# Optimization experiments

Measured on AMD Instinct MI355X. Metric: run time of the kernel, lower is better.

## Reference

```python
import jax, jax.numpy as jnp
import numpy as np

NUM_JOINTS = 24
NUM_THETAS = NUM_JOINTS * 3  # 72
NUM_VERTS = 6890
NUM_BETAS = 10
BATCH = 512

SMPL_PARENTS = np.array([0, 0, 0, 0, 1, 2, 3, 4, 5, 6, 7, 8, 9, 9, 9,
                         12, 13, 14, 16, 17, 18, 19, 20, 21], dtype=np.int32)


def setup_inputs() -> dict:
    key = jax.random.key(0)
    ks = jax.random.split(key, 6)
    x = jax.random.normal(ks[0], (BATCH, NUM_THETAS + NUM_BETAS), dtype=jnp.float32) * 0.3
    v_template = jax.random.normal(ks[1], (NUM_VERTS, 3), dtype=jnp.float32) * 0.3
    shapedirs = jax.random.normal(ks[2], (NUM_BETAS, NUM_VERTS * 3), dtype=jnp.float32) * 0.01
    posedirs = jax.random.normal(ks[3], (207, NUM_VERTS * 3), dtype=jnp.float32) * 0.001
    Jr = jax.random.uniform(ks[4], (NUM_VERTS, NUM_JOINTS), dtype=jnp.float32)
    J_regressor = Jr / jnp.sum(Jr, axis=0, keepdims=True)
    W = jax.random.uniform(ks[5], (NUM_VERTS, NUM_JOINTS), dtype=jnp.float32)
    lbs_weights = W / jnp.sum(W, axis=1, keepdims=True)  # rows sum to 1 (skinning weights)
    parents = jnp.asarray(SMPL_PARENTS)
    return {"x": x, "v_template": v_template, "shapedirs": shapedirs,
            "J_regressor": J_regressor, "posedirs": posedirs,
            "lbs_weights": lbs_weights, "parents": parents}


def batch_rodrigues(theta):
    # theta: [N,3] axis-angle -> [N,3,3] rotation matrices
    angle = jnp.linalg.norm(theta + 1e-8, axis=1, keepdims=True)  # [N,1]
    r = theta / angle                                              # [N,3] unit axis
    cos = jnp.cos(angle)[..., None]                                # [N,1,1]
    sin = jnp.sin(angle)[..., None]
    outer = r[:, :, None] * r[:, None, :]                          # [N,3,3]
    rx, ry, rz = r[:, 0], r[:, 1], r[:, 2]
    zero = jnp.zeros_like(rx)
    K = jnp.stack([zero, -rz, ry,
                   rz, zero, -rx,
                   -ry, rx, zero], axis=1).reshape(-1, 3, 3)       # skew-symmetric
    eye = jnp.eye(3, dtype=theta.dtype)
    return cos * eye + (1.0 - cos) * outer + sin * K


def global_rigid_transformation(Rs, J, parents):
    # Rs: [B,24,3,3], J: [B,24,3] -> A: [B,24,4,4]
    B = Rs.shape[0]
    dtype = Rs.dtype
    bottom = jnp.broadcast_to(jnp.array([0, 0, 0, 1], dtype=dtype), (B, 1, 4))

    def make_A(R, t):  # R:[B,3,3], t:[B,3]
        Rt = jnp.concatenate([R, t[:, :, None]], axis=2)  # [B,3,4]
        return jnp.concatenate([Rt, bottom], axis=1)       # [B,4,4]

    parents = np.asarray(parents)
    results = [make_A(Rs[:, 0], J[:, 0])]
    for i in range(1, NUM_JOINTS):
        t_rel = J[:, i] - J[:, parents[i]]
        A_here = make_A(Rs[:, i], t_rel)
        results.append(jnp.matmul(results[parents[i]], A_here))
    results = jnp.stack(results, axis=1)  # [B,24,4,4]

    Js_w0 = jnp.concatenate([J, jnp.zeros((B, NUM_JOINTS, 1), dtype=dtype)], axis=2)  # [B,24,4]
    init_bone = jnp.einsum('bjpq,bjq->bjp', results, Js_w0)                           # [B,24,4]
    A = results - jnp.pad(init_bone[..., None], ((0, 0), (0, 0), (0, 0), (3, 0)))
    return A


def reference(x, v_template, shapedirs, J_regressor, posedirs, lbs_weights, parents):
    B = x.shape[0]
    thetas = x[:, :NUM_THETAS]
    betas = x[:, NUM_THETAS:]

    # shape blendshapes
    v_shaped = (betas @ shapedirs).reshape(B, NUM_VERTS, 3) + v_template  # [B,V,3]

    J = jnp.einsum('bvc,vj->bjc', v_shaped, J_regressor)  # [B,24,3]

    # pose rotations + pose blendshapes
    Rs = batch_rodrigues(thetas.reshape(-1, 3)).reshape(B, NUM_JOINTS, 3, 3)
    pose_feature = (Rs[:, 1:] - jnp.eye(3, dtype=x.dtype)).reshape(B, 207)
    v_posed = (pose_feature @ posedirs).reshape(B, NUM_VERTS, 3) + v_shaped

    # kinematic chain
    A = global_rigid_transformation(Rs, J, parents)  # [B,24,4,4]

    # linear blend skinning
    T = jnp.einsum('vj,bjpq->bvpq', lbs_weights, A)  # [B,V,4,4]
    v_posed_homo = jnp.concatenate(
        [v_posed, jnp.ones((B, NUM_VERTS, 1), dtype=x.dtype)], axis=2)  # [B,V,4]
    verts = jnp.einsum('bvpq,bvq->bvp', T, v_posed_homo)[:, :, :3]
    return verts
```

## Files before the change

kernel.cpp:

```cpp
#include <hip/hip_runtime.h>

#define NUM_JOINTS 24
#define NUM_VERTS  6890
#define NUM_COORDS (NUM_VERTS * 3)
#define NUM_BETAS  10
#define KTOT       217
#define KPAD       224
#define BATCH      512
#define VPAD       6912

#define WS_SJP  0
#define WS_XBF  85536
#define WS_DBF  142880
#define WS_WHBF 2465312
#define WS_AH   2575904
#define WS_AL   2706976

typedef __attribute__((ext_vector_type(8))) short short8;
typedef __attribute__((ext_vector_type(4))) float f32x4;

__device__ inline unsigned short f2bf(float f) {
    union { float f; unsigned u; } c; c.f = f;
    unsigned u = c.u;
    u += 0x7fffu + ((u >> 16) & 1u);
    return (unsigned short)(u >> 16);
}
__device__ inline float bf2f(unsigned short h) {
    union { unsigned u; float f; } c; c.u = ((unsigned)h) << 16;
    return c.f;
}

struct PBShm {
    float Rs[4][24][9];
    float Jl[4][24][3];
    float Rg[4][24][9];
    float tg[4][24][3];
    float As[4][24][12];
};

__global__ __launch_bounds__(256) void k_prep(const float* __restrict__ Jr,
                                              const float* __restrict__ sd,
                                              const float* __restrict__ pd,
                                              const float* __restrict__ vt,
                                              const float* __restrict__ w,
                                              float* __restrict__ ws) {
    __shared__ __align__(16) unsigned char smem[28928];
    const int t   = blockIdx.x;
    const int tid = threadIdx.x;
    unsigned short* whbf = (unsigned short*)(ws + WS_WHBF);
    unsigned short* dbf  = (unsigned short*)(ws + WS_DBF);

    if (t < 27) {
        const int v = t * 256 + tid;
        const bool ok = (v < NUM_VERTS);
        unsigned short row[32];
        #pragma unroll
        for (int j = 0; j < 32; ++j)
            row[j] = f2bf((ok && j < 24) ? w[v * 24 + j] : 0.f);
        #pragma unroll
        for (int i = 0; i < 4; ++i)
            *(float4*)(whbf + (size_t)v * 32 + i * 8) = *(const float4*)(&row[i * 8]);
    } else if (t < 351) {
        unsigned* L = (unsigned*)smem;
        const int c0   = (t - 27) * 64;
        const int lane = tid & 63;
        const int grp  = tid >> 6;
        const int c    = c0 + lane;
        const bool cv  = (c < NUM_COORDS);
        #pragma unroll 4
        for (int i = 0; i < 28; ++i) {
            const int p  = i * 4 + grp;
            const int k0 = 2 * p, k1 = k0 + 1;
            float v0 = 0.f, v1 = 0.f;
            if (cv) {
                v0 = (k0 < 10) ? sd[(size_t)k0 * NUM_COORDS + c]
                   : (k0 < KTOT) ? pd[(size_t)(k0 - 10) * NUM_COORDS + c] : 0.f;
                v1 = (k1 < 10) ? sd[(size_t)k1 * NUM_COORDS + c]
                   : (k1 < KTOT) ? pd[(size_t)(k1 - 10) * NUM_COORDS + c] : 0.f;
            }
            L[lane * 113 + p] = (unsigned)f2bf(v0) | ((unsigned)f2bf(v1) << 16);
        }
        __syncthreads();
        #pragma unroll
        for (int i = 0; i < 7; ++i) {
            const int idx = i * 256 + tid;
            const int row = idx / 28;
            const int q   = idx % 28;
            uint4 val;
            val.x = L[row * 113 + q * 4 + 0];
            val.y = L[row * 113 + q * 4 + 1];
            val.z = L[row * 113 + q * 4 + 2];
            val.w = L[row * 113 + q * 4 + 3];
            *(uint4*)(dbf + (size_t)(c0 + row) * KPAD + q * 8) = val;
        }
    } else {
        float* Jl = (float*)smem;
        float* S  = (float*)smem + 64 * 25;
        const int strip = t - 351;
        const int v0 = strip * 64;
        #pragma unroll
        for (int i = 0; i < 6; ++i) {
            const int idx = i * 256 + tid;
            const int v = idx / 24, j = idx % 24;
            Jl[v * 25 + j] = (v0 + v < NUM_VERTS) ? Jr[(size_t)(v0 + v) * 24 + j] : 0.f;
        }
        #pragma unroll
        for (int i = 0; i < 9; ++i) {
            const int idx = i * 256 + tid;
            if (idx < 33 * 64) {
                const int s = idx / 64, v = idx % 64;
                float val = 0.f;
                if (v0 + v < NUM_VERTS) {
                    if (s < 30) val = sd[(size_t)(s / 3) * NUM_COORDS + (size_t)(v0 + v) * 3 + (s % 3)];
                    else        val = vt[(size_t)(v0 + v) * 3 + (s - 30)];
                }
                S[s * 64 + v] = val;
            }
        }
        __syncthreads();
        float* wsp = ws + WS_SJP + (size_t)strip * 792;
        for (int o = tid; o < 792; o += 256) {
            const int s = o / 24, j = o % 24;
            float sum = 0.f;
            #pragma unroll 8
            for (int v = 0; v < 64; ++v)
                sum += S[s * 64 + v] * Jl[v * 25 + j];
            wsp[o] = sum;
        }
    }
}

__global__ __launch_bounds__(256) void k_pb(const float* __restrict__ x,
                                            const int* __restrict__ parents,
                                            float* __restrict__ ws) {
    __shared__ PBShm P;
    __shared__ float SJf[792];
    unsigned short* xbf = (unsigned short*)(ws + WS_XBF);
    unsigned short* ahi = (unsigned short*)(ws + WS_AH);
    unsigned short* alo = (unsigned short*)(ws + WS_AL);
    const int tid = threadIdx.x;

    {
        const float* wsp = ws + WS_SJP;
        for (int o = tid; o < 792; o += 256) {
            float sum = 0.f;
            for (int s2 = 0; s2 < 108; ++s2)
                sum += wsp[(size_t)s2 * 792 + o];
            SJf[o] = sum;
        }
    }
    __syncthreads();

    const int sub  = tid >> 6;
    const int lane = tid & 63;
    const int b = blockIdx.x * 4 + sub;
    const float* row = x + b * (NUM_BETAS + 72);

    if (lane < 24) {
        const int j = lane;
        const float t0 = row[3 * j + 0], t1 = row[3 * j + 1], t2 = row[3 * j + 2];
        const float a0 = t0 + 1e-8f, a1 = t1 + 1e-8f, a2 = t2 + 1e-8f;
        const float angle = sqrtf(a0 * a0 + a1 * a1 + a2 * a2);
        const float inv = 1.0f / angle;
        const float rx = t0 * inv, ry = t1 * inv, rz = t2 * inv;
        const float c = cosf(angle), sn = sinf(angle), o = 1.f - c;
        float R[9];
        R[0] = c + o * rx * rx;       R[1] = o * rx * ry - sn * rz; R[2] = o * rx * rz + sn * ry;
        R[3] = o * rx * ry + sn * rz; R[4] = c + o * ry * ry;       R[5] = o * ry * rz - sn * rx;
        R[6] = o * rx * rz - sn * ry; R[7] = o * ry * rz + sn * rx; R[8] = c + o * rz * rz;
        #pragma unroll
        for (int i = 0; i < 9; ++i) P.Rs[sub][j][i] = R[i];
        #pragma unroll
        for (int c3 = 0; c3 < 3; ++c3) {
            float s = SJf[(30 + c3) * 24 + j];
            #pragma unroll
            for (int k = 0; k < NUM_BETAS; ++k)
                s += row[72 + k] * SJf[(k * 3 + c3) * 24 + j];
            P.Jl[sub][j][c3] = s;
        }
        if (j >= 1) {
            #pragma unroll
            for (int i = 0; i < 9; ++i) {
                const float pf = R[i] - ((i == 0 || i == 4 || i == 8) ? 1.f : 0.f);
                xbf[(size_t)b * KPAD + 10 + (j - 1) * 9 + i] = f2bf(pf);
            }
        }
    }
    if (lane < NUM_BETAS) xbf[(size_t)b * KPAD + lane] = f2bf(row[72 + lane]);
    if (lane == 63) {
        #pragma unroll
        for (int k = KTOT; k < KPAD; ++k) xbf[(size_t)b * KPAD + k] = 0;
    }
    __syncthreads();

    if (lane == 0) {
        float Rg[24][9], tg[24][3];
        #pragma unroll
        for (int q = 0; q < 9; ++q) { Rg[0][q] = P.Rs[sub][0][q]; P.Rg[sub][0][q] = Rg[0][q]; }
        #pragma unroll
        for (int c3 = 0; c3 < 3; ++c3) { tg[0][c3] = P.Jl[sub][0][c3]; P.tg[sub][0][c3] = tg[0][c3]; }

        #pragma unroll
        for (int i = 1; i < 24; ++i) {
            constexpr int PAR[24] = {0, 0, 0, 0, 1, 2, 3, 4, 5, 6, 7, 8,
                                     9, 9, 9, 12, 13, 14, 16, 17, 18, 19, 20, 21};
            const int p = PAR[i];
            float Rsl[9];
            #pragma unroll
            for (int q = 0; q < 9; ++q) Rsl[q] = P.Rs[sub][i][q];
            float tmp[9];
            #pragma unroll
            for (int r = 0; r < 3; ++r)
                #pragma unroll
                for (int cc = 0; cc < 3; ++cc)
                    tmp[r * 3 + cc] = Rg[p][r * 3 + 0] * Rsl[0 + cc] +
                                      Rg[p][r * 3 + 1] * Rsl[3 + cc] +
                                      Rg[p][r * 3 + 2] * Rsl[6 + cc];
            #pragma unroll
            for (int q = 0; q < 9; ++q) { Rg[i][q] = tmp[q]; P.Rg[sub][i][q] = tmp[q]; }
            const float tr0 = P.Jl[sub][i][0] - P.Jl[sub][p][0];
            const float tr1 = P.Jl[sub][i][1] - P.Jl[sub][p][1];
            const float tr2 = P.Jl[sub][i][2] - P.Jl[sub][p][2];
            #pragma unroll
            for (int r = 0; r < 3; ++r) {
                tg[i][r] = Rg[p][r * 3 + 0] * tr0 + Rg[p][r * 3 + 1] * tr1 +
                           Rg[p][r * 3 + 2] * tr2 + tg[p][r];
                P.tg[sub][i][r] = tg[i][r];
            }
        }
    }
    __syncthreads();

    if (lane < 24) {
        const int j = lane;
        #pragma unroll
        for (int r = 0; r < 3; ++r) {
            const float tt = P.tg[sub][j][r] - (P.Rg[sub][j][r * 3 + 0] * P.Jl[sub][j][0] +
                                                P.Rg[sub][j][r * 3 + 1] * P.Jl[sub][j][1] +
                                                P.Rg[sub][j][r * 3 + 2] * P.Jl[sub][j][2]);
            P.As[sub][j][r * 4 + 0] = P.Rg[sub][j][r * 3 + 0];
            P.As[sub][j][r * 4 + 1] = P.Rg[sub][j][r * 3 + 1];
            P.As[sub][j][r * 4 + 2] = P.Rg[sub][j][r * 3 + 2];
            P.As[sub][j][r * 4 + 3] = tt;
        }
    }
    __syncthreads();

    if (lane < 32) {
        const int r = lane >> 1;
        const int half = lane & 1;
        unsigned short hi[16], lo[16];
        #pragma unroll
        for (int i = 0; i < 16; ++i) {
            const int j = half * 16 + i;
            float v = 0.f;
            if (r < 12 && j < 24) v = P.As[sub][j][r];
            const unsigned short h = f2bf(v);
            hi[i] = h;
            lo[i] = f2bf(v - bf2f(h));
        }
        unsigned short* dh = ahi + ((size_t)b * 16 + r) * 32 + half * 16;
        unsigned short* dl = alo + ((size_t)b * 16 + r) * 32 + half * 16;
        #pragma unroll
        for (int i = 0; i < 2; ++i) {
            *(float4*)(dh + i * 8) = *(const float4*)(&hi[i * 8]);
            *(float4*)(dl + i * 8) = *(const float4*)(&lo[i * 8]);
        }
    }
}

__global__ __launch_bounds__(256) void k_fused(const float* __restrict__ vt,
                                               float* __restrict__ out,
                                               float* __restrict__ ws) {
    __shared__ __align__(16) float VP[64 * 194];
    __shared__ __align__(16) unsigned char U[20480];
    unsigned short* Xs = (unsigned short*)U;
    float*          Tsf = (float*)U;

    const unsigned short* dbf  = (const unsigned short*)(ws + WS_DBF);
    const unsigned short* xbf  = (const unsigned short*)(ws + WS_XBF);
    const unsigned short* whbf = (const unsigned short*)(ws + WS_WHBF);
    const unsigned short* ahi  = (const unsigned short*)(ws + WS_AH);
    const unsigned short* alo  = (const unsigned short*)(ws + WS_AL);

    const int tid  = threadIdx.x;
    const int wave = tid >> 6;
    const int lane = tid & 63;
    const int col  = lane & 15;
    const int quad = lane >> 4;
    const int c0   = blockIdx.x * 192;
    const int b0   = blockIdx.y * 64;

    short8 bfrag[3][7];
    float vtl[3];
    #pragma unroll
    for (int nt = 0; nt < 3; ++nt) {
        const int nc = c0 + wave * 48 + nt * 16 + col;
        const unsigned short* brow = dbf + (size_t)nc * KPAD + quad * 8;
        #pragma unroll
        for (int kb = 0; kb < 7; ++kb)
            bfrag[nt][kb] = *(const short8*)(brow + kb * 32);
        vtl[nt] = (nc < NUM_COORDS) ? vt[nc] : 0.f;
    }

    for (int chunk = 0; chunk < 2; ++chunk) {
        const int m0 = b0 + chunk * 32;
        __syncthreads();
        #pragma unroll
        for (int i = 0; i < 4; ++i) {
            const int c = tid + i * 256;
            if (c < 32 * 28) {
                const int r = c / 28, off = c % 28;
                *(float4*)(&Xs[r * 232 + off * 8]) =
                    *(const float4*)(xbf + (size_t)(m0 + r) * KPAD + off * 8);
            }
        }
        __syncthreads();

        #pragma unroll
        for (int mt = 0; mt < 2; ++mt) {
            const unsigned short* arow = &Xs[(mt * 16 + col) * 232 + quad * 8];
            f32x4 acc[3] = {{0.f,0.f,0.f,0.f},{0.f,0.f,0.f,0.f},{0.f,0.f,0.f,0.f}};
            #pragma unroll
            for (int kb = 0; kb < 7; ++kb) {
                const short8 af = *(const short8*)(arow + kb * 32);
                #pragma unroll
                for (int nt = 0; nt < 3; ++nt)
                    acc[nt] = __builtin_amdgcn_mfma_f32_16x16x32_bf16(af, bfrag[nt][kb], acc[nt], 0, 0, 0);
            }
            #pragma unroll
            for (int nt = 0; nt < 3; ++nt) {
                const int cc = wave * 48 + nt * 16 + col;
                #pragma unroll
                for (int r = 0; r < 4; ++r)
                    VP[(chunk * 32 + mt * 16 + quad * 4 + r) * 194 + cc] = acc[nt][r] + vtl[nt];
            }
        }
    }
    __syncthreads();

    const int v0 = blockIdx.x * 64;
    short8 wfrag[4];
    #pragma unroll
    for (int mt = 0; mt < 4; ++mt)
        wfrag[mt] = *(const short8*)(whbf + (size_t)(v0 + mt * 16 + col) * 32 + quad * 8);

    float* ts = Tsf + wave * (64 * 20);
    const int vv = v0 + lane;
    const bool vok = (vv < NUM_VERTS);

    for (int nt = wave; nt < 64; nt += 4) {
        const int b = b0 + nt;
        const short8 bh = *(const short8*)(ahi + ((size_t)b * 16 + col) * 32 + quad * 8);
        const short8 bl = *(const short8*)(alo + ((size_t)b * 16 + col) * 32 + quad * 8);

        f32x4 acc2[4];
        #pragma unroll
        for (int mt = 0; mt < 4; ++mt) {
            f32x4 z = {0.f, 0.f, 0.f, 0.f};
            z = __builtin_amdgcn_mfma_f32_16x16x32_bf16(wfrag[mt], bh, z, 0, 0, 0);
            z = __builtin_amdgcn_mfma_f32_16x16x32_bf16(wfrag[mt], bl, z, 0, 0, 0);
            acc2[mt] = z;
        }
        #pragma unroll
        for (int mt = 0; mt < 4; ++mt)
            #pragma unroll
            for (int r = 0; r < 4; ++r)
                ts[(mt * 16 + quad * 4 + r) * 20 + col] = acc2[mt][r];

        const f32x4 t0 = *(const f32x4*)(ts + lane * 20 + 0);
        const f32x4 t1 = *(const f32x4*)(ts + lane * 20 + 4);
        const f32x4 t2 = *(const f32x4*)(ts + lane * 20 + 8);

        const float h0 = VP[nt * 194 + lane * 3 + 0];
        const float h1 = VP[nt * 194 + lane * 3 + 1];
        const float h2 = VP[nt * 194 + lane * 3 + 2];

        if (vok) {
            float* orow = out + (size_t)b * NUM_COORDS + (size_t)vv * 3;
            __builtin_nontemporal_store(t0[0] * h0 + t0[1] * h1 + t0[2] * h2 + t0[3], orow + 0);
            __builtin_nontemporal_store(t1[0] * h0 + t1[1] * h1 + t1[2] * h2 + t1[3], orow + 1);
            __builtin_nontemporal_store(t2[0] * h0 + t2[1] * h1 + t2[2] * h2 + t2[3], orow + 2);
        }
    }
}

extern "C" void kernel_launch(void* const* d_in, const int* in_sizes, int n_in,
                              void* d_out, int out_size, void* d_ws, size_t ws_size,
                              hipStream_t stream) {
    const float* x  = (const float*)d_in[0];
    const float* vt = (const float*)d_in[1];
    const float* sd = (const float*)d_in[2];
    const float* Jr = (const float*)d_in[3];
    const float* pd = (const float*)d_in[4];
    const float* w  = (const float*)d_in[5];
    const int* parents = (const int*)d_in[6];
    float* out = (float*)d_out;
    float* ws  = (float*)d_ws;

    k_prep <<<459, 256, 0, stream>>>(Jr, sd, pd, vt, w, ws);
    k_pb   <<<128, 256, 0, stream>>>(x, parents, ws);
    k_fused<<<dim3(108, 8), 256, 0, stream>>>(vt, out, ws);
}
```

Baseline: 156.1 us.

## Merge three kernels into one cooperative persistent kernel with grid syncs

Replaces the three separate launches (prep, per-batch kinematics, fused GEMM/skinning) with a single cooperative kernel that loops over the original block indices and uses grid-wide syncs between phases. The aim is to remove launch overhead and inter-kernel gaps. In exchange the kernel carries one 70 KB shared-memory allocation and a launch bound of two blocks per CU. The grid is capped at 512 blocks, so the 864 GEMM tiles run in a strided loop with less parallelism per phase, and the grid syncs add their own cost.

```diff
diff --git a/kernel.cpp b/kernel.cpp
--- a/kernel.cpp
+++ b/kernel.cpp
@@ -1,4 +1,7 @@
 #include <hip/hip_runtime.h>
+#include <hip/hip_cooperative_groups.h>
+
+namespace cg = cooperative_groups;
 
 #define NUM_JOINTS 24
 #define NUM_VERTS  6890
@@ -38,349 +41,364 @@
     float As[4][24][12];
 };
 
-__global__ __launch_bounds__(256) void k_prep(const float* __restrict__ Jr,
-                                              const float* __restrict__ sd,
-                                              const float* __restrict__ pd,
-                                              const float* __restrict__ vt,
-                                              const float* __restrict__ w,
-                                              float* __restrict__ ws) {
-    __shared__ __align__(16) unsigned char smem[28928];
-    const int t   = blockIdx.x;
+__global__ __launch_bounds__(256, 2) void k_mega(const float* __restrict__ Jr,
+                                                 const float* __restrict__ sd,
+                                                 const float* __restrict__ pd,
+                                                 const float* __restrict__ vt,
+                                                 const float* __restrict__ w,
+                                                 const float* __restrict__ x,
+                                                 const int* __restrict__ parents,
+                                                 float* __restrict__ out,
+                                                 float* __restrict__ ws) {
+    cg::grid_group grid = cg::this_grid();
+    __shared__ __align__(16) unsigned char SMEM[70144];
     const int tid = threadIdx.x;
-    unsigned short* whbf = (unsigned short*)(ws + WS_WHBF);
-    unsigned short* dbf  = (unsigned short*)(ws + WS_DBF);
-
-    if (t < 27) {
-        const int v = t * 256 + tid;
-        const bool ok = (v < NUM_VERTS);
-        unsigned short row[32];
-        #pragma unroll
-        for (int j = 0; j < 32; ++j)
-            row[j] = f2bf((ok && j < 24) ? w[v * 24 + j] : 0.f);
-        #pragma unroll
-        for (int i = 0; i < 4; ++i)
-            *(float4*)(whbf + (size_t)v * 32 + i * 8) = *(const float4*)(&row[i * 8]);
-    } else if (t < 351) {
-        unsigned* L = (unsigned*)smem;
-        const int c0   = (t - 27) * 64;
-        const int lane = tid & 63;
-        const int grp  = tid >> 6;
-        const int c    = c0 + lane;
-        const bool cv  = (c < NUM_COORDS);
-        #pragma unroll 4
-        for (int i = 0; i < 28; ++i) {
-            const int p  = i * 4 + grp;
-            const int k0 = 2 * p, k1 = k0 + 1;
-            float v0 = 0.f, v1 = 0.f;
-            if (cv) {
-                v0 = (k0 < 10) ? sd[(size_t)k0 * NUM_COORDS + c]
-                   : (k0 < KTOT) ? pd[(size_t)(k0 - 10) * NUM_COORDS + c] : 0.f;
-                v1 = (k1 < 10) ? sd[(size_t)k1 * NUM_COORDS + c]
-                   : (k1 < KTOT) ? pd[(size_t)(k1 - 10) * NUM_COORDS + c] : 0.f;
-            }
-            L[lane * 113 + p] = (unsigned)f2bf(v0) | ((unsigned)f2bf(v1) << 16);
-        }
+    const int bx  = blockIdx.x;
+    const int nbk = gridDim.x;
+
+    for (int t = bx; t < 459; t += nbk) {
         __syncthreads();
-        #pragma unroll
-        for (int i = 0; i < 7; ++i) {
-            const int idx = i * 256 + tid;
-            const int row = idx / 28;
-            const int q   = idx % 28;
-            uint4 val;
-            val.x = L[row * 113 + q * 4 + 0];
-            val.y = L[row * 113 + q * 4 + 1];
-            val.z = L[row * 113 + q * 4 + 2];
-            val.w = L[row * 113 + q * 4 + 3];
-            *(uint4*)(dbf + (size_t)(c0 + row) * KPAD + q * 8) = val;
-        }
-    } else {
-        float* Jl = (float*)smem;
-        float* S  = (float*)smem + 64 * 25;
-        const int strip = t - 351;
-        const int v0 = strip * 64;
-        #pragma unroll
-        for (int i = 0; i < 6; ++i) {
-            const int idx = i * 256 + tid;
-            const int v = idx / 24, j = idx % 24;
-            Jl[v * 25 + j] = (v0 + v < NUM_VERTS) ? Jr[(size_t)(v0 + v) * 24 + j] : 0.f;
-        }
-        #pragma unroll
-        for (int i = 0; i < 9; ++i) {
-            const int idx = i * 256 + tid;
-            if (idx < 33 * 64) {
-                const int s = idx / 64, v = idx % 64;
-                float val = 0.f;
-                if (v0 + v < NUM_VERTS) {
-                    if (s < 30) val = sd[(size_t)(s / 3) * NUM_COORDS + (size_t)(v0 + v) * 3 + (s % 3)];
-                    else        val = vt[(size_t)(v0 + v) * 3 + (s - 30)];
-                }
-                S[s * 64 + v] = val;
-            }
-        }
-        __syncthreads();
-        float* wsp = ws + WS_SJP + (size_t)strip * 792;
-        for (int o = tid; o < 792; o += 256) {
-            const int s = o / 24, j = o % 24;
-            float sum = 0.f;
-            #pragma unroll 8
-            for (int v = 0; v < 64; ++v)
-                sum += S[s * 64 + v] * Jl[v * 25 + j];
-            wsp[o] = sum;
+        unsigned short* whbf = (unsigned short*)(ws + WS_WHBF);
+        unsigned short* dbf  = (unsigned short*)(ws + WS_DBF);
+
+        if (t < 27) {
+            const int v = t * 256 + tid;
+            const bool ok = (v < NUM_VERTS);
+            unsigned short row[32];
+            #pragma unroll
+            for (int j = 0; j < 32; ++j)
+                row[j] = f2bf((ok && j < 24) ? w[v * 24 + j] : 0.f);
+            #pragma unroll
+            for (int i = 0; i < 4; ++i)
+                *(float4*)(whbf + (size_t)v * 32 + i * 8) = *(const float4*)(&row[i * 8]);
+        } else if (t < 351) {
+            unsigned* L = (unsigned*)SMEM;
+            const int c0   = (t - 27) * 64;
+            const int lane = tid & 63;
+            const int grp  = tid >> 6;
+            const int c    = c0 + lane;
+            const bool cv  = (c < NUM_COORDS);
+            #pragma unroll 4
+            for (int i = 0; i < 28; ++i) {
+                const int p  = i * 4 + grp;
+                const int k0 = 2 * p, k1 = k0 + 1;
+                float v0 = 0.f, v1 = 0.f;
+                if (cv) {
+                    v0 = (k0 < 10) ? sd[(size_t)k0 * NUM_COORDS + c]
+                       : (k0 < KTOT) ? pd[(size_t)(k0 - 10) * NUM_COORDS + c] : 0.f;
+                    v1 = (k1 < 10) ? sd[(size_t)k1 * NUM_COORDS + c]
+                       : (k1 < KTOT) ? pd[(size_t)(k1 - 10) * NUM_COORDS + c] : 0.f;
+                }
+                L[lane * 113 + p] = (unsigned)f2bf(v0) | ((unsigned)f2bf(v1) << 16);
+            }
+            __syncthreads();
+            #pragma unroll
+            for (int i = 0; i < 7; ++i) {
+                const int idx = i * 256 + tid;
+                const int row = idx / 28;
+                const int q   = idx % 28;
+                uint4 val;
+                val.x = L[row * 113 + q * 4 + 0];
+                val.y = L[row * 113 + q * 4 + 1];
+                val.z = L[row * 113 + q * 4 + 2];
+                val.w = L[row * 113 + q * 4 + 3];
+                *(uint4*)(dbf + (size_t)(c0 + row) * KPAD + q * 8) = val;
+            }
+        } else {
+            float* Jl = (float*)SMEM;
+            float* S  = (float*)SMEM + 64 * 25;
+            const int strip = t - 351;
+            const int v0 = strip * 64;
+            #pragma unroll
+            for (int i = 0; i < 6; ++i) {
+                const int idx = i * 256 + tid;
+                const int v = idx / 24, j = idx % 24;
+                Jl[v * 25 + j] = (v0 + v < NUM_VERTS) ? Jr[(size_t)(v0 + v) * 24 + j] : 0.f;
+            }
+            #pragma unroll
+            for (int i = 0; i < 9; ++i) {
+                const int idx = i * 256 + tid;
+                if (idx < 33 * 64) {
+                    const int s = idx / 64, v = idx % 64;
+                    float val = 0.f;
+                    if (v0 + v < NUM_VERTS) {
+                        if (s < 30) val = sd[(size_t)(s / 3) * NUM_COORDS + (size_t)(v0 + v) * 3 + (s % 3)];
+                        else        val = vt[(size_t)(v0 + v) * 3 + (s - 30)];
+                    }
+                    S[s * 64 + v] = val;
+                }
+            }
+            __syncthreads();
+            float* wsp = ws + WS_SJP + (size_t)strip * 792;
+            for (int o = tid; o < 792; o += 256) {
+                const int s = o / 24, j = o % 24;
+                float sum = 0.f;
+                #pragma unroll 8
+                for (int v = 0; v < 64; ++v)
+                    sum += S[s * 64 + v] * Jl[v * 25 + j];
+                wsp[o] = sum;
+            }
         }
     }
-}
-
-__global__ __launch_bounds__(256) void k_pb(const float* __restrict__ x,
-                                            const int* __restrict__ parents,
-                                            float* __restrict__ ws) {
-    __shared__ PBShm P;
-    __shared__ float SJf[792];
-    unsigned short* xbf = (unsigned short*)(ws + WS_XBF);
-    unsigned short* ahi = (unsigned short*)(ws + WS_AH);
-    unsigned short* alo = (unsigned short*)(ws + WS_AL);
-    const int tid = threadIdx.x;
-
-    {
-        const float* wsp = ws + WS_SJP;
-        for (int o = tid; o < 792; o += 256) {
-            float sum = 0.f;
-            for (int s2 = 0; s2 < 108; ++s2)
-                sum += wsp[(size_t)s2 * 792 + o];
-            SJf[o] = sum;
+
+    grid.sync();
+
+    if (bx < 128) {
+        PBShm* P   = (PBShm*)SMEM;
+        float* SJf = (float*)(SMEM + sizeof(PBShm));
+        unsigned short* xbf = (unsigned short*)(ws + WS_XBF);
+        unsigned short* ahi = (unsigned short*)(ws + WS_AH);
+        unsigned short* alo = (unsigned short*)(ws + WS_AL);
+
+        for (int pbb = bx; pbb < 128; pbb += nbk) {
+            __syncthreads();
+            {
+                const float* wsp = ws + WS_SJP;
+                for (int o = tid; o < 792; o += 256) {
+                    float sum = 0.f;
+                    for (int s2 = 0; s2 < 108; ++s2)
+                        sum += wsp[(size_t)s2 * 792 + o];
+                    SJf[o] = sum;
+                }
+            }
+            __syncthreads();
+
+            const int sub  = tid >> 6;
+            const int lane = tid & 63;
+            const int b = pbb * 4 + sub;
+            const float* row = x + b * (NUM_BETAS + 72);
+
+            if (lane < 24) {
+                const int j = lane;
+                const float t0 = row[3 * j + 0], t1 = row[3 * j + 1], t2 = row[3 * j + 2];
+                const float a0 = t0 + 1e-8f, a1 = t1 + 1e-8f, a2 = t2 + 1e-8f;
+                const float angle = sqrtf(a0 * a0 + a1 * a1 + a2 * a2);
+                const float inv = 1.0f / angle;
+                const float rx = t0 * inv, ry = t1 * inv, rz = t2 * inv;
+                const float c = cosf(angle), sn = sinf(angle), o = 1.f - c;
+                float R[9];
+                R[0] = c + o * rx * rx;       R[1] = o * rx * ry - sn * rz; R[2] = o * rx * rz + sn * ry;
+                R[3] = o * rx * ry + sn * rz; R[4] = c + o * ry * ry;       R[5] = o * ry * rz - sn * rx;
+                R[6] = o * rx * rz - sn * ry; R[7] = o * ry * rz + sn * rx; R[8] = c + o * rz * rz;
+                #pragma unroll
+                for (int i = 0; i < 9; ++i) P->Rs[sub][j][i] = R[i];
+                #pragma unroll
+                for (int c3 = 0; c3 < 3; ++c3) {
+                    float s = SJf[(30 + c3) * 24 + j];
+                    #pragma unroll
+                    for (int k = 0; k < NUM_BETAS; ++k)
+                        s += row[72 + k] * SJf[(k * 3 + c3) * 24 + j];
+                    P->Jl[sub][j][c3] = s;
+                }
+                if (j >= 1) {
+                    #pragma unroll
+                    for (int i = 0; i < 9; ++i) {
+                        const float pf = R[i] - ((i == 0 || i == 4 || i == 8) ? 1.f : 0.f);
+                        xbf[(size_t)b * KPAD + 10 + (j - 1) * 9 + i] = f2bf(pf);
+                    }
+                }
+            }
+            if (lane < NUM_BETAS) xbf[(size_t)b * KPAD + lane] = f2bf(row[72 + lane]);
+            if (lane == 63) {
+                #pragma unroll
+                for (int k = KTOT; k < KPAD; ++k) xbf[(size_t)b * KPAD + k] = 0;
+            }
+            __syncthreads();
+
+            if (lane == 0) {
+                float Rg[24][9], tg[24][3];
+                #pragma unroll
+                for (int q = 0; q < 9; ++q) { Rg[0][q] = P->Rs[sub][0][q]; P->Rg[sub][0][q] = Rg[0][q]; }
+                #pragma unroll
+                for (int c3 = 0; c3 < 3; ++c3) { tg[0][c3] = P->Jl[sub][0][c3]; P->tg[sub][0][c3] = tg[0][c3]; }
+
+                #pragma unroll
+                for (int i = 1; i < 24; ++i) {
+                    constexpr int PAR[24] = {0, 0, 0, 0, 1, 2, 3, 4, 5, 6, 7, 8,
+                                             9, 9, 9, 12, 13, 14, 16, 17, 18, 19, 20, 21};
+                    const int p = PAR[i];
+                    float Rsl[9];
+                    #pragma unroll
+                    for (int q = 0; q < 9; ++q) Rsl[q] = P->Rs[sub][i][q];
+                    float tmp[9];
+                    #pragma unroll
+                    for (int r = 0; r < 3; ++r)
+                        #pragma unroll
+                        for (int cc = 0; cc < 3; ++cc)
+                            tmp[r * 3 + cc] = Rg[p][r * 3 + 0] * Rsl[0 + cc] +
+                                              Rg[p][r * 3 + 1] * Rsl[3 + cc] +
+                                              Rg[p][r * 3 + 2] * Rsl[6 + cc];
+                    #pragma unroll
+                    for (int q = 0; q < 9; ++q) { Rg[i][q] = tmp[q]; P->Rg[sub][i][q] = tmp[q]; }
+                    const float tr0 = P->Jl[sub][i][0] - P->Jl[sub][p][0];
+                    const float tr1 = P->Jl[sub][i][1] - P->Jl[sub][p][1];
+                    const float tr2 = P->Jl[sub][i][2] - P->Jl[sub][p][2];
+                    #pragma unroll
+                    for (int r = 0; r < 3; ++r) {
+                        tg[i][r] = Rg[p][r * 3 + 0] * tr0 + Rg[p][r * 3 + 1] * tr1 +
+                                   Rg[p][r * 3 + 2] * tr2 + tg[p][r];
+                        P->tg[sub][i][r] = tg[i][r];
+                    }
+                }
+            }
+            __syncthreads();
+
+            if (lane < 24) {
+                const int j = lane;
+                #pragma unroll
+                for (int r = 0; r < 3; ++r) {
+                    const float tt = P->tg[sub][j][r] - (P->Rg[sub][j][r * 3 + 0] * P->Jl[sub][j][0] +
+                                                        P->Rg[sub][j][r * 3 + 1] * P->Jl[sub][j][1] +
+                                                        P->Rg[sub][j][r * 3 + 2] * P->Jl[sub][j][2]);
+                    P->As[sub][j][r * 4 + 0] = P->Rg[sub][j][r * 3 + 0];
+                    P->As[sub][j][r * 4 + 1] = P->Rg[sub][j][r * 3 + 1];
+                    P->As[sub][j][r * 4 + 2] = P->Rg[sub][j][r * 3 + 2];
+                    P->As[sub][j][r * 4 + 3] = tt;
+                }
+            }
+            __syncthreads();
+
+            if (lane < 32) {
+                const int r = lane >> 1;
+                const int half = lane & 1;
+                unsigned short hi[16], lo[16];
+                #pragma unroll
+                for (int i = 0; i < 16; ++i) {
+                    const int j = half * 16 + i;
+                    float v = 0.f;
+                    if (r < 12 && j < 24) v = P->As[sub][j][r];
+                    const unsigned short h = f2bf(v);
+                    hi[i] = h;
+                    lo[i] = f2bf(v - bf2f(h));
+                }
+                unsigned short* dh = ahi + ((size_t)b * 16 + r) * 32 + half * 16;
+                unsigned short* dl = alo + ((size_t)b * 16 + r) * 32 + half * 16;
+                #pragma unroll
+                for (int i = 0; i < 2; ++i) {
+                    *(float4*)(dh + i * 8) = *(const float4*)(&hi[i * 8]);
+                    *(float4*)(dl + i * 8) = *(const float4*)(&lo[i * 8]);
+                }
+            }
         }
     }
-    __syncthreads();
-
-    const int sub  = tid >> 6;
-    const int lane = tid & 63;
-    const int b = blockIdx.x * 4 + sub;
-    const float* row = x + b * (NUM_BETAS + 72);
-
-    if (lane < 24) {
-        const int j = lane;
-        const float t0 = row[3 * j + 0], t1 = row[3 * j + 1], t2 = row[3 * j + 2];
-        const float a0 = t0 + 1e-8f, a1 = t1 + 1e-8f, a2 = t2 + 1e-8f;
-        const float angle = sqrtf(a0 * a0 + a1 * a1 + a2 * a2);
-        const float inv = 1.0f / angle;
-        const float rx = t0 * inv, ry = t1 * inv, rz = t2 * inv;
-        const float c = cosf(angle), sn = sinf(angle), o = 1.f - c;
-        float R[9];
-        R[0] = c + o * rx * rx;       R[1] = o * rx * ry - sn * rz; R[2] = o * rx * rz + sn * ry;
-        R[3] = o * rx * ry + sn * rz; R[4] = c + o * ry * ry;       R[5] = o * ry * rz - sn * rx;
-        R[6] = o * rx * rz - sn * ry; R[7] = o * ry * rz + sn * rx; R[8] = c + o * rz * rz;
-        #pragma unroll
-        for (int i = 0; i < 9; ++i) P.Rs[sub][j][i] = R[i];
-        #pragma unroll
-        for (int c3 = 0; c3 < 3; ++c3) {
-            float s = SJf[(30 + c3) * 24 + j];
-            #pragma unroll
-            for (int k = 0; k < NUM_BETAS; ++k)
-                s += row[72 + k] * SJf[(k * 3 + c3) * 24 + j];
-            P.Jl[sub][j][c3] = s;
-        }
-        if (j >= 1) {
-            #pragma unroll
-            for (int i = 0; i < 9; ++i) {
-                const float pf = R[i] - ((i == 0 || i == 4 || i == 8) ? 1.f : 0.f);
-                xbf[(size_t)b * KPAD + 10 + (j - 1) * 9 + i] = f2bf(pf);
-            }
-        }
-    }
-    if (lane < NUM_BETAS) xbf[(size_t)b * KPAD + lane] = f2bf(row[72 + lane]);
-    if (lane == 63) {
-        #pragma unroll
-        for (int k = KTOT; k < KPAD; ++k) xbf[(size_t)b * KPAD + k] = 0;
-    }
-    __syncthreads();
-
-    if (lane == 0) {
-        float Rg[24][9], tg[24][3];
-        #pragma unroll
-        for (int q = 0; q < 9; ++q) { Rg[0][q] = P.Rs[sub][0][q]; P.Rg[sub][0][q] = Rg[0][q]; }
-        #pragma unroll
-        for (int c3 = 0; c3 < 3; ++c3) { tg[0][c3] = P.Jl[sub][0][c3]; P.tg[sub][0][c3] = tg[0][c3]; }
-
-        #pragma unroll
-        for (int i = 1; i < 24; ++i) {
-            constexpr int PAR[24] = {0, 0, 0, 0, 1, 2, 3, 4, 5, 6, 7, 8,
-                                     9, 9, 9, 12, 13, 14, 16, 17, 18, 19, 20, 21};
-            const int p = PAR[i];
-            float Rsl[9];
-            #pragma unroll
-            for (int q = 0; q < 9; ++q) Rsl[q] = P.Rs[sub][i][q];
-            float tmp[9];
-            #pragma unroll
-            for (int r = 0; r < 3; ++r)
-                #pragma unroll
-                for (int cc = 0; cc < 3; ++cc)
-                    tmp[r * 3 + cc] = Rg[p][r * 3 + 0] * Rsl[0 + cc] +
-                                      Rg[p][r * 3 + 1] * Rsl[3 + cc] +
-                                      Rg[p][r * 3 + 2] * Rsl[6 + cc];
-            #pragma unroll
-            for (int q = 0; q < 9; ++q) { Rg[i][q] = tmp[q]; P.Rg[sub][i][q] = tmp[q]; }
-            const float tr0 = P.Jl[sub][i][0] - P.Jl[sub][p][0];
-            const float tr1 = P.Jl[sub][i][1] - P.Jl[sub][p][1];
-            const float tr2 = P.Jl[sub][i][2] - P.Jl[sub][p][2];
-            #pragma unroll
-            for (int r = 0; r < 3; ++r) {
-                tg[i][r] = Rg[p][r * 3 + 0] * tr0 + Rg[p][r * 3 + 1] * tr1 +
-                           Rg[p][r * 3 + 2] * tr2 + tg[p][r];
-                P.tg[sub][i][r] = tg[i][r];
-            }
-        }
-    }
-    __syncthreads();
-
-    if (lane < 24) {
-        const int j = lane;
-        #pragma unroll
-        for (int r = 0; r < 3; ++r) {
-            const float tt = P.tg[sub][j][r] - (P.Rg[sub][j][r * 3 + 0] * P.Jl[sub][j][0] +
-                                                P.Rg[sub][j][r * 3 + 1] * P.Jl[sub][j][1] +
-                                                P.Rg[sub][j][r * 3 + 2] * P.Jl[sub][j][2]);
-            P.As[sub][j][r * 4 + 0] = P.Rg[sub][j][r * 3 + 0];
-            P.As[sub][j][r * 4 + 1] = P.Rg[sub][j][r * 3 + 1];
-            P.As[sub][j][r * 4 + 2] = P.Rg[sub][j][r * 3 + 2];
-            P.As[sub][j][r * 4 + 3] = tt;
-        }
-    }
-    __syncthreads();
-
-    if (lane < 32) {
-        const int r = lane >> 1;
-        const int half = lane & 1;
-        unsigned short hi[16], lo[16];
-        #pragma unroll
-        for (int i = 0; i < 16; ++i) {
-            const int j = half * 16 + i;
-            float v = 0.f;
-            if (r < 12 && j < 24) v = P.As[sub][j][r];
-            const unsigned short h = f2bf(v);
-            hi[i] = h;
-            lo[i] = f2bf(v - bf2f(h));
-        }
-        unsigned short* dh = ahi + ((size_t)b * 16 + r) * 32 + half * 16;
-        unsigned short* dl = alo + ((size_t)b * 16 + r) * 32 + half * 16;
-        #pragma unroll
-        for (int i = 0; i < 2; ++i) {
-            *(float4*)(dh + i * 8) = *(const float4*)(&hi[i * 8]);
-            *(float4*)(dl + i * 8) = *(const float4*)(&lo[i * 8]);
-        }
-    }
-}
-
-__global__ __launch_bounds__(256) void k_fused(const float* __restrict__ vt,
-                                               float* __restrict__ out,
-                                               float* __restrict__ ws) {
-    __shared__ __align__(16) float VP[64 * 194];
-    __shared__ __align__(16) unsigned char U[20480];
-    unsigned short* Xs = (unsigned short*)U;
-    float*          Tsf = (float*)U;
-
-    const unsigned short* dbf  = (const unsigned short*)(ws + WS_DBF);
-    const unsigned short* xbf  = (const unsigned short*)(ws + WS_XBF);
-    const unsigned short* whbf = (const unsigned short*)(ws + WS_WHBF);
-    const unsigned short* ahi  = (const unsigned short*)(ws + WS_AH);
-    const unsigned short* alo  = (const unsigned short*)(ws + WS_AL);
-
-    const int tid  = threadIdx.x;
-    const int wave = tid >> 6;
-    const int lane = tid & 63;
-    const int col  = lane & 15;
-    const int quad = lane >> 4;
-    const int c0   = blockIdx.x * 192;
-    const int b0   = blockIdx.y * 64;
-
-    short8 bfrag[3][7];
-    float vtl[3];
-    #pragma unroll
-    for (int nt = 0; nt < 3; ++nt) {
-        const int nc = c0 + wave * 48 + nt * 16 + col;
-        const unsigned short* brow = dbf + (size_t)nc * KPAD + quad * 8;
-        #pragma unroll
-        for (int kb = 0; kb < 7; ++kb)
-            bfrag[nt][kb] = *(const short8*)(brow + kb * 32);
-        vtl[nt] = (nc < NUM_COORDS) ? vt[nc] : 0.f;
-    }
-
-    for (int chunk = 0; chunk < 2; ++chunk) {
-        const int m0 = b0 + chunk * 32;
-        __syncthreads();
-        #pragma unroll
-        for (int i = 0; i < 4; ++i) {
-            const int c = tid + i * 256;
-            if (c < 32 * 28) {
-                const int r = c / 28, off = c % 28;
-                *(float4*)(&Xs[r * 232 + off * 8]) =
-                    *(const float4*)(xbf + (size_t)(m0 + r) * KPAD + off * 8);
-            }
-        }
-        __syncthreads();
-
-        #pragma unroll
-        for (int mt = 0; mt < 2; ++mt) {
-            const unsigned short* arow = &Xs[(mt * 16 + col) * 232 + quad * 8];
-            f32x4 acc[3] = {{0.f,0.f,0.f,0.f},{0.f,0.f,0.f,0.f},{0.f,0.f,0.f,0.f}};
-            #pragma unroll
-            for (int kb = 0; kb < 7; ++kb) {
-                const short8 af = *(const short8*)(arow + kb * 32);
-                #pragma unroll
-                for (int nt = 0; nt < 3; ++nt)
-                    acc[nt] = __builtin_amdgcn_mfma_f32_16x16x32_bf16(af, bfrag[nt][kb], acc[nt], 0, 0, 0);
-            }
+
+    grid.sync();
+
+    {
+        float* VP = (float*)SMEM;
+        unsigned char* U = SMEM + 64 * 194 * 4;
+        unsigned short* Xs  = (unsigned short*)U;
+        float*          Tsf = (float*)U;
+
+        const unsigned short* dbf  = (const unsigned short*)(ws + WS_DBF);
+        const unsigned short* xbf  = (const unsigned short*)(ws + WS_XBF);
+        const unsigned short* whbf = (const unsigned short*)(ws + WS_WHBF);
+        const unsigned short* ahi  = (const unsigned short*)(ws + WS_AH);
+        const unsigned short* alo  = (const unsigned short*)(ws + WS_AL);
+
+        const int wave = tid >> 6;
+        const int lane = tid & 63;
+        const int col  = lane & 15;
+        const int quad = lane >> 4;
+
+        for (int tile = bx; tile < 864; tile += nbk) {
+            const int bxx = tile % 108;
+            const int byy = tile / 108;
+            const int c0  = bxx * 192;
+            const int b0  = byy * 64;
+
+            short8 bfrag[3][7];
+            float vtl[3];
             #pragma unroll
             for (int nt = 0; nt < 3; ++nt) {
-                const int cc = wave * 48 + nt * 16 + col;
-                #pragma unroll
-                for (int r = 0; r < 4; ++r)
-                    VP[(chunk * 32 + mt * 16 + quad * 4 + r) * 194 + cc] = acc[nt][r] + vtl[nt];
-            }
-        }
-    }
-    __syncthreads();
-
-    const int v0 = blockIdx.x * 64;
-    short8 wfrag[4];
-    #pragma unroll
-    for (int mt = 0; mt < 4; ++mt)
-        wfrag[mt] = *(const short8*)(whbf + (size_t)(v0 + mt * 16 + col) * 32 + quad * 8);
-
-    float* ts = Tsf + wave * (64 * 20);
-    const int vv = v0 + lane;
-    const bool vok = (vv < NUM_VERTS);
-
-    for (int nt = wave; nt < 64; nt += 4) {
-        const int b = b0 + nt;
-        const short8 bh = *(const short8*)(ahi + ((size_t)b * 16 + col) * 32 + quad * 8);
-        const short8 bl = *(const short8*)(alo + ((size_t)b * 16 + col) * 32 + quad * 8);
-
-        f32x4 acc2[4];
-        #pragma unroll
-        for (int mt = 0; mt < 4; ++mt) {
-            f32x4 z = {0.f, 0.f, 0.f, 0.f};
-            z = __builtin_amdgcn_mfma_f32_16x16x32_bf16(wfrag[mt], bh, z, 0, 0, 0);
-            z = __builtin_amdgcn_mfma_f32_16x16x32_bf16(wfrag[mt], bl, z, 0, 0, 0);
-            acc2[mt] = z;
-        }
-        #pragma unroll
-        for (int mt = 0; mt < 4; ++mt)
-            #pragma unroll
-            for (int r = 0; r < 4; ++r)
-                ts[(mt * 16 + quad * 4 + r) * 20 + col] = acc2[mt][r];
-
-        const f32x4 t0 = *(const f32x4*)(ts + lane * 20 + 0);
-        const f32x4 t1 = *(const f32x4*)(ts + lane * 20 + 4);
-        const f32x4 t2 = *(const f32x4*)(ts + lane * 20 + 8);
-
-        const float h0 = VP[nt * 194 + lane * 3 + 0];
-        const float h1 = VP[nt * 194 + lane * 3 + 1];
-        const float h2 = VP[nt * 194 + lane * 3 + 2];
-
-        if (vok) {
-            float* orow = out + (size_t)b * NUM_COORDS + (size_t)vv * 3;
-            __builtin_nontemporal_store(t0[0] * h0 + t0[1] * h1 + t0[2] * h2 + t0[3], orow + 0);
-            __builtin_nontemporal_store(t1[0] * h0 + t1[1] * h1 + t1[2] * h2 + t1[3], orow + 1);
-            __builtin_nontemporal_store(t2[0] * h0 + t2[1] * h1 + t2[2] * h2 + t2[3], orow + 2);
+                const int nc = c0 + wave * 48 + nt * 16 + col;
+                const unsigned short* brow = dbf + (size_t)nc * KPAD + quad * 8;
+                #pragma unroll
+                for (int kb = 0; kb < 7; ++kb)
+                    bfrag[nt][kb] = *(const short8*)(brow + kb * 32);
+                vtl[nt] = (nc < NUM_COORDS) ? vt[nc] : 0.f;
+            }
+
+            for (int chunk = 0; chunk < 2; ++chunk) {
+                const int m0 = b0 + chunk * 32;
+                __syncthreads();
+                #pragma unroll
+                for (int i = 0; i < 4; ++i) {
+                    const int c = tid + i * 256;
+                    if (c < 32 * 28) {
+                        const int r = c / 28, off = c % 28;
+                        *(float4*)(&Xs[r * 232 + off * 8]) =
+                            *(const float4*)(xbf + (size_t)(m0 + r) * KPAD + off * 8);
+                    }
+                }
+                __syncthreads();
+
+                #pragma unroll
+                for (int mt = 0; mt < 2; ++mt) {
+                    const unsigned short* arow = &Xs[(mt * 16 + col) * 232 + quad * 8];
+                    f32x4 acc[3] = {{0.f,0.f,0.f,0.f},{0.f,0.f,0.f,0.f},{0.f,0.f,0.f,0.f}};
+                    #pragma unroll
+                    for (int kb = 0; kb < 7; ++kb) {
+                        const short8 af = *(const short8*)(arow + kb * 32);
+                        #pragma unroll
+                        for (int nt = 0; nt < 3; ++nt)
+                            acc[nt] = __builtin_amdgcn_mfma_f32_16x16x32_bf16(af, bfrag[nt][kb], acc[nt], 0, 0, 0);
+                    }
+                    #pragma unroll
+                    for (int nt = 0; nt < 3; ++nt) {
+                        const int cc = wave * 48 + nt * 16 + col;
+                        #pragma unroll
+                        for (int r = 0; r < 4; ++r)
+                            VP[(chunk * 32 + mt * 16 + quad * 4 + r) * 194 + cc] = acc[nt][r] + vtl[nt];
+                    }
+                }
+            }
+            __syncthreads();
+
+            const int v0 = bxx * 64;
+            short8 wfrag[4];
+            #pragma unroll
+            for (int mt = 0; mt < 4; ++mt)
+                wfrag[mt] = *(const short8*)(whbf + (size_t)(v0 + mt * 16 + col) * 32 + quad * 8);
+
+            float* ts = Tsf + wave * (64 * 20);
+            const int vv = v0 + lane;
+            const bool vok = (vv < NUM_VERTS);
+
+            for (int nt = wave; nt < 64; nt += 4) {
+                const int b = b0 + nt;
+                const short8 bh = *(const short8*)(ahi + ((size_t)b * 16 + col) * 32 + quad * 8);
+                const short8 bl = *(const short8*)(alo + ((size_t)b * 16 + col) * 32 + quad * 8);
+
+                f32x4 acc2[4];
+                #pragma unroll
+                for (int mt = 0; mt < 4; ++mt) {
+                    f32x4 z = {0.f, 0.f, 0.f, 0.f};
+                    z = __builtin_amdgcn_mfma_f32_16x16x32_bf16(wfrag[mt], bh, z, 0, 0, 0);
+                    z = __builtin_amdgcn_mfma_f32_16x16x32_bf16(wfrag[mt], bl, z, 0, 0, 0);
+                    acc2[mt] = z;
+                }
+                #pragma unroll
+                for (int mt = 0; mt < 4; ++mt)
+                    #pragma unroll
+                    for (int r = 0; r < 4; ++r)
+                        ts[(mt * 16 + quad * 4 + r) * 20 + col] = acc2[mt][r];
+
+                const f32x4 t0 = *(const f32x4*)(ts + lane * 20 + 0);
+                const f32x4 t1 = *(const f32x4*)(ts + lane * 20 + 4);
+                const f32x4 t2 = *(const f32x4*)(ts + lane * 20 + 8);
+
+                const float h0 = VP[nt * 194 + lane * 3 + 0];
+                const float h1 = VP[nt * 194 + lane * 3 + 1];
+                const float h2 = VP[nt * 194 + lane * 3 + 2];
+
+                if (vok) {
+                    float* orow = out + (size_t)b * NUM_COORDS + (size_t)vv * 3;
+                    __builtin_nontemporal_store(t0[0] * h0 + t0[1] * h1 + t0[2] * h2 + t0[3], orow + 0);
+                    __builtin_nontemporal_store(t1[0] * h0 + t1[1] * h1 + t1[2] * h2 + t1[3], orow + 1);
+                    __builtin_nontemporal_store(t2[0] * h0 + t2[1] * h1 + t2[2] * h2 + t2[3], orow + 2);
+                }
+            }
         }
     }
 }
@@ -398,7 +416,18 @@
     float* out = (float*)d_out;
     float* ws  = (float*)d_ws;
 
-    k_prep <<<459, 256, 0, stream>>>(Jr, sd, pd, vt, w, ws);
-    k_pb   <<<128, 256, 0, stream>>>(x, parents, ws);
-    k_fused<<<dim3(108, 8), 256, 0, stream>>>(vt, out, ws);
+    static int coop_grid = 0;
+    if (coop_grid == 0) {
+        int nb = 0;
+        hipOccupancyMaxActiveBlocksPerMultiprocessor(&nb, k_mega, 256, 0);
+        if (nb < 1) nb = 1;
+        int g = nb * 256;
+        coop_grid = (g > 512) ? 512 : g;
+        if (coop_grid < 128) coop_grid = 128;
+    }
+
+    void* args[] = { (void*)&Jr, (void*)&sd, (void*)&pd, (void*)&vt, (void*)&w,
+                     (void*)&x, (void*)&parents, (void*)&out, (void*)&ws };
+    hipLaunchCooperativeKernel((void*)k_mega, dim3(coop_grid), dim3(256),
+                               args, 0, stream);
 }
```

Measured after the change: 257.9 us. +65.2%, slower.
